# Kernel tuning notes

Hardware: AMD Instinct MI355X
Metric: run time of the kernel (lower is better)

The kernel has to match this reference:

```python
import jax, jax.numpy as jnp
import numpy as np

N_NODES = 100000
N_EDGES = 1000000
HID = 128


def setup_inputs() -> dict:
    key = jax.random.key(0)
    ks = jax.random.split(key, 13)
    s = 0.05  # small init scale for numerical sanity
    return {
        "z": jax.random.normal(ks[0], (N_NODES, HID), jnp.float32),
        "edge": jax.random.randint(ks[1], (N_EDGES, 2), 0, N_NODES, jnp.int64),
        # hadamard_mlp: Linear(HID -> HID//2), ReLU, Linear(HID//2 -> 1)
        "w_h1": jax.random.normal(ks[2], (HID // 2, HID), jnp.float32) * s,
        "b_h1": jax.random.normal(ks[3], (HID // 2,), jnp.float32) * s,
        "w_h2": jax.random.normal(ks[4], (1, HID // 2), jnp.float32) * s,
        "b_h2": jax.random.normal(ks[5], (1,), jnp.float32) * s,
        # concat_mlp: Linear(2*HID -> HID), ReLU, Linear(HID -> 1)
        "w_c1": jax.random.normal(ks[6], (HID, 2 * HID), jnp.float32) * s,
        "b_c1": jax.random.normal(ks[7], (HID,), jnp.float32) * s,
        "w_c2": jax.random.normal(ks[8], (1, HID), jnp.float32) * s,
        "b_c2": jax.random.normal(ks[9], (1,), jnp.float32) * s,
        # bilinear: weight [1, HID, HID], bias [1]
        "w_b": jax.random.normal(ks[10], (1, HID, HID), jnp.float32) * s,
        "b_b": jax.random.normal(ks[11], (1,), jnp.float32) * s,
        "strategy_weights": jnp.ones((3,), jnp.float32) / 3.0,
    }


def reference(z, edge, w_h1, b_h1, w_h2, b_h2, w_c1, b_c1, w_c2, b_c2,
              w_b, b_b, strategy_weights):
    src, dst = edge[:, 0], edge[:, 1]
    z_src = z[src]                      # [E, D] gather
    z_dst = z[dst]                      # [E, D] gather
    w = jax.nn.softmax(strategy_weights)

    # strategy 1: hadamard MLP (dropout is identity in eval)
    had = z_src * z_dst                 # [E, D]
    h = jax.nn.relu(jnp.einsum('ed,hd->eh', had, w_h1) + b_h1)
    score1 = (jnp.einsum('eh,oh->eo', h, w_h2) + b_h2)[:, 0]

    # strategy 2: concat MLP
    cat = jnp.concatenate([z_src, z_dst], axis=1)  # [E, 2D]
    c = jax.nn.relu(jnp.einsum('ed,hd->eh', cat, w_c1) + b_c1)
    score2 = (jnp.einsum('eh,oh->eo', c, w_c2) + b_c2)[:, 0]

    # strategy 3: bilinear  out_e = z_src_e^T W z_dst_e + b
    score3 = jnp.einsum('ed,df,ef->e', z_src, w_b[0], z_dst) + b_b[0]

    return w[0] * score1 + w[1] * score2 + w[2] * score3
```

## Files before the change

kernel.cpp:

```cpp
#include <hip/hip_runtime.h>
#include <hip/hip_bf16.h>

#define N_NODES 100000
#define N_EDGES 1000000
#define SRCB 384
#define DSTB 512
#define NB (N_EDGES / 16)

typedef float f32x4 __attribute__((ext_vector_type(4)));
typedef float f32x2 __attribute__((ext_vector_type(2)));
typedef _Float16 f16x8 __attribute__((ext_vector_type(8)));
typedef _Float16 f16x2 __attribute__((ext_vector_type(2)));

__device__ inline f16x8 pack8(float4 a, float4 b) {
    f16x8 o;
    o[0] = (_Float16)a.x; o[1] = (_Float16)a.y; o[2] = (_Float16)a.z; o[3] = (_Float16)a.w;
    o[4] = (_Float16)b.x; o[5] = (_Float16)b.y; o[6] = (_Float16)b.z; o[7] = (_Float16)b.w;
    return o;
}
__device__ inline void mfma16(f32x4& acc, f16x8 a, f16x8 b) {
    acc = __builtin_amdgcn_mfma_f32_16x16x32_f16(a, b, acc, 0, 0, 0);
}
__device__ inline float fdot2(f16x8 a, f16x8 b, int j2, float c) {
    f16x2 pa = { a[2 * j2], a[2 * j2 + 1] };
    f16x2 pb = { b[2 * j2], b[2 * j2 + 1] };
    return __builtin_amdgcn_fdot2(pa, pb, c, false);
}
__device__ inline unsigned char f2fp8(float v) {
    int p = __builtin_amdgcn_cvt_pk_fp8_f32(v, v, 0, false);
    return (unsigned char)(p & 0xff);
}

__global__ __launch_bounds__(256) void precomp_kernel(
    const float* __restrict__ z, const float* __restrict__ w_c1,
    const float* __restrict__ b_c1, const float* __restrict__ w_b,
    unsigned char* __restrict__ Ps8, unsigned char* __restrict__ Pd8)
{
    const int lane = threadIdx.x & 63;
    const int r = lane & 15, g = lane >> 4;
    const int wid = blockIdx.x * 4 + (threadIdx.x >> 6);
    const int ct = wid % 6;
    const int walker = wid / 6;
    const int nWalk = (gridDim.x * 4) / 6;
    if (walker >= nWalk) return;

    f16x8 bw[4][4];
#pragma unroll
    for (int nt = 0; nt < 4; ++nt) {
        const int c = ct * 64 + nt * 16 + r;
        const float* wrow;
        if (c < 128)       wrow = w_c1 + (size_t)c * 256;
        else if (c < 256)  wrow = w_c1 + (size_t)(c - 128) * 256 + 128;
        else               wrow = w_b + (size_t)(c - 256) * 128;
#pragma unroll
        for (int kk = 0; kk < 4; ++kk) {
            const int k0 = kk * 32 + g * 8;
            float4 f0 = *reinterpret_cast<const float4*>(wrow + k0);
            float4 f1 = *reinterpret_cast<const float4*>(wrow + k0 + 4);
            bw[nt][kk] = pack8(f0, f1);
        }
    }
    float bc1v[4] = {0.f, 0.f, 0.f, 0.f};
    if (ct < 2) {
#pragma unroll
        for (int nt = 0; nt < 4; ++nt) bc1v[nt] = b_c1[ct * 64 + nt * 16 + r];
    }

    for (int nb = walker; nb < N_NODES / 16; nb += nWalk) {
        const float* zp = z + (size_t)(nb * 16 + r) * 128;
        f32x4 acc[4] = {};
#pragma unroll
        for (int kk = 0; kk < 4; ++kk) {
            const int k0 = kk * 32 + g * 8;
            float4 z0 = *reinterpret_cast<const float4*>(zp + k0);
            float4 z1 = *reinterpret_cast<const float4*>(zp + k0 + 4);
            f16x8 a = pack8(z0, z1);
#pragma unroll
            for (int nt = 0; nt < 4; ++nt) mfma16(acc[nt], a, bw[nt][kk]);
        }
#pragma unroll
        for (int nt = 0; nt < 4; ++nt) {
#pragma unroll
            for (int rr = 0; rr < 4; ++rr) {
                const float v = acc[nt][rr] + bc1v[nt];
                const int node = nb * 16 + g * 4 + rr;
                const int c = ct * 64 + nt * 16 + r;
                if (ct < 2) {
                    Ps8[(size_t)node * SRCB + c] = f2fp8(v);
                } else if (ct < 4) {
                    Pd8[(size_t)node * DSTB + (c - 128)] = f2fp8(v);
                } else {
                    *reinterpret_cast<_Float16*>(
                        Pd8 + (size_t)node * DSTB + 128 + (size_t)(c - 256) * 2)
                        = (_Float16)v;
                }
            }
        }
    }
}

__global__ __launch_bounds__(256) void zb_kernel(const float* __restrict__ z,
                                                 unsigned char* __restrict__ Ps8,
                                                 unsigned char* __restrict__ Pd8)
{
    const int i = blockIdx.x * 256 + threadIdx.x;
    if (i >= N_NODES * 16) return;
    const int node = i >> 4, ch = i & 15;
    const float* zp = z + (size_t)node * 128 + ch * 8;
    float4 a = *reinterpret_cast<const float4*>(zp);
    float4 b = *reinterpret_cast<const float4*>(zp + 4);
    *reinterpret_cast<f16x8*>(Ps8 + (size_t)node * SRCB + 128 + ch * 16) = pack8(a, b);
    int w0 = __builtin_amdgcn_cvt_pk_fp8_f32(a.x, a.y, 0, false);
    w0 = __builtin_amdgcn_cvt_pk_fp8_f32(a.z, a.w, w0, true);
    int w1 = __builtin_amdgcn_cvt_pk_fp8_f32(b.x, b.y, 0, false);
    w1 = __builtin_amdgcn_cvt_pk_fp8_f32(b.z, b.w, w1, true);
    uint2 pk; pk.x = (unsigned)w0; pk.y = (unsigned)w1;
    *reinterpret_cast<uint2*>(Pd8 + (size_t)node * DSTB + 384 + ch * 8) = pk;
}

__global__ __launch_bounds__(256) void edge_kernel(
    const int2* __restrict__ edge2,
    const unsigned char* __restrict__ Ps8, const unsigned char* __restrict__ Pd8,
    const float* __restrict__ w_h1, const float* __restrict__ b_h1,
    const float* __restrict__ w_h2, const float* __restrict__ b_h2,
    const float* __restrict__ w_c2, const float* __restrict__ b_c2,
    const float* __restrict__ b_b, const float* __restrict__ sw,
    float* __restrict__ out)
{
    __shared__ f16x8 bwlds[1024];

    const int tid = threadIdx.x;
    for (int e = tid; e < 1024; e += 256) {
        const int r_ = e & 15, g_ = (e >> 4) & 3, kkf = (e >> 6) & 3, ntf = e >> 8;
        const float* wr = w_h1 + (size_t)(ntf * 16 + r_) * 128 + g_ * 32 + kkf * 8;
        float4 f0 = *reinterpret_cast<const float4*>(wr);
        float4 f1 = *reinterpret_cast<const float4*>(wr + 4);
        bwlds[e] = pack8(f0, f1);
    }
    __syncthreads();

    const int lane = tid & 63;
    const int r = lane & 15, g = lane >> 4;

    const float s0 = sw[0], s1 = sw[1], s2 = sw[2];
    const float mx = fmaxf(s0, fmaxf(s1, s2));
    const float e0 = __expf(s0 - mx), e1 = __expf(s1 - mx), e2 = __expf(s2 - mx);
    const float inv = 1.0f / (e0 + e1 + e2);
    const float W0 = e0 * inv, W1 = e1 * inv, W2 = e2 * inv;
    const float cbias = W0 * b_h2[0] + W1 * b_c2[0] + W2 * b_b[0];

    float bh1v[4], wh2v[4];
#pragma unroll
    for (int nt = 0; nt < 4; ++nt) {
        bh1v[nt] = b_h1[nt * 16 + r];
        wh2v[nt] = w_h2[nt * 16 + r] * W0;
    }
    f16x8 wc2r[4];
#pragma unroll
    for (int kk = 0; kk < 4; ++kk) {
        const int k0 = g * 32 + kk * 8;
        float4 f0 = *reinterpret_cast<const float4*>(w_c2 + k0);
        float4 f1 = *reinterpret_cast<const float4*>(w_c2 + k0 + 4);
        f0.x *= W1; f0.y *= W1; f0.z *= W1; f0.w *= W1;
        f1.x *= W1; f1.y *= W1; f1.z *= W1; f1.w *= W1;
        wc2r[kk] = pack8(f0, f1);
    }
    const f16x8* myb = bwlds + g * 16 + r;

    const int gwid = (blockIdx.x * blockDim.x + tid) >> 6;
    const int nW = (gridDim.x * blockDim.x) >> 6;
    const int rsel = r & 3;
    const int srcl = ((r >> 2) << 4) | r;

    int b = gwid;
    int2 sd = make_int2(0, 0);
    if (b < NB) sd = edge2[b * 16 + r];

    for (; b < NB; b += nW) {
        const int bn = b + nW;
        int2 sdn = sd;
        if (bn < NB) sdn = edge2[bn * 16 + r];

        const int base = b * 16;
        const unsigned char* ps = Ps8 + (size_t)sd.x * SRCB;
        const unsigned char* pd = Pd8 + (size_t)sd.y * DSTB;

        uint4 a16[2], b16[2], zq[2];
        f16x8 zs[4], yv[4];
        a16[0] = *reinterpret_cast<const uint4*>(ps + g * 32);
        a16[1] = *reinterpret_cast<const uint4*>(ps + g * 32 + 16);
        b16[0] = *reinterpret_cast<const uint4*>(pd + g * 32);
        b16[1] = *reinterpret_cast<const uint4*>(pd + g * 32 + 16);
        zq[0]  = *reinterpret_cast<const uint4*>(pd + 384 + g * 32);
        zq[1]  = *reinterpret_cast<const uint4*>(pd + 384 + g * 32 + 16);
#pragma unroll
        for (int kk = 0; kk < 4; ++kk) {
            const int of = g * 64 + kk * 16;
            zs[kk] = *reinterpret_cast<const f16x8*>(ps + 128 + of);
            yv[kk] = *reinterpret_cast<const f16x8*>(pd + 128 + of);
        }
        const unsigned zdw[8] = { zq[0].x, zq[0].y, zq[0].z, zq[0].w,
                                  zq[1].x, zq[1].y, zq[1].z, zq[1].w };

        f32x4 acc[4] = {};
#pragma unroll
        for (int kk = 0; kk < 4; ++kk) {
            f32x2 p0 = __builtin_amdgcn_cvt_pk_f32_fp8((int)zdw[2 * kk], false);
            f32x2 p1 = __builtin_amdgcn_cvt_pk_f32_fp8((int)zdw[2 * kk], true);
            f32x2 p2 = __builtin_amdgcn_cvt_pk_f32_fp8((int)zdw[2 * kk + 1], false);
            f32x2 p3 = __builtin_amdgcn_cvt_pk_f32_fp8((int)zdw[2 * kk + 1], true);
            f16x8 a;
            a[0] = (_Float16)((float)zs[kk][0] * p0.x);
            a[1] = (_Float16)((float)zs[kk][1] * p0.y);
            a[2] = (_Float16)((float)zs[kk][2] * p1.x);
            a[3] = (_Float16)((float)zs[kk][3] * p1.y);
            a[4] = (_Float16)((float)zs[kk][4] * p2.x);
            a[5] = (_Float16)((float)zs[kk][5] * p2.y);
            a[6] = (_Float16)((float)zs[kk][6] * p3.x);
            a[7] = (_Float16)((float)zs[kk][7] * p3.y);
            mfma16(acc[0], a, myb[(0 * 4 + kk) * 64]);
            mfma16(acc[1], a, myb[(1 * 4 + kk) * 64]);
            mfma16(acc[2], a, myb[(2 * 4 + kk) * 64]);
            mfma16(acc[3], a, myb[(3 * 4 + kk) * 64]);
        }
        float t4[4];
#pragma unroll
        for (int rr = 0; rr < 4; ++rr) {
            float s = 0.f;
#pragma unroll
            for (int nt = 0; nt < 4; ++nt)
                s = fmaf(fmaxf(acc[nt][rr] + bh1v[nt], 0.f), wh2v[nt], s);
            t4[rr] = s;
        }
#pragma unroll
        for (int mask = 1; mask <= 8; mask <<= 1) {
#pragma unroll
            for (int rr = 0; rr < 4; ++rr)
                t4[rr] += __shfl_xor(t4[rr], mask, 16);
        }
        float u = t4[0];
        if (rsel == 1) u = t4[1];
        if (rsel == 2) u = t4[2];
        if (rsel == 3) u = t4[3];
        const float sc1w = __shfl(u, srcl, 64);

        float sA = 0.f, sB = 0.f;
#pragma unroll
        for (int h = 0; h < 2; ++h) {
            const unsigned ax = a16[h].x, ay = a16[h].y, az = a16[h].z, aw = a16[h].w;
            const unsigned bx = b16[h].x, by = b16[h].y, bz = b16[h].z, bw_ = b16[h].w;
            f32x2 pa0 = __builtin_amdgcn_cvt_pk_f32_fp8((int)ax, false);
            f32x2 pa1 = __builtin_amdgcn_cvt_pk_f32_fp8((int)ax, true);
            f32x2 pa2 = __builtin_amdgcn_cvt_pk_f32_fp8((int)ay, false);
            f32x2 pa3 = __builtin_amdgcn_cvt_pk_f32_fp8((int)ay, true);
            f32x2 pa4 = __builtin_amdgcn_cvt_pk_f32_fp8((int)az, false);
            f32x2 pa5 = __builtin_amdgcn_cvt_pk_f32_fp8((int)az, true);
            f32x2 pa6 = __builtin_amdgcn_cvt_pk_f32_fp8((int)aw, false);
            f32x2 pa7 = __builtin_amdgcn_cvt_pk_f32_fp8((int)aw, true);
            f32x2 pb0 = __builtin_amdgcn_cvt_pk_f32_fp8((int)bx, false);
            f32x2 pb1 = __builtin_amdgcn_cvt_pk_f32_fp8((int)bx, true);
            f32x2 pb2 = __builtin_amdgcn_cvt_pk_f32_fp8((int)by, false);
            f32x2 pb3 = __builtin_amdgcn_cvt_pk_f32_fp8((int)by, true);
            f32x2 pb4 = __builtin_amdgcn_cvt_pk_f32_fp8((int)bz, false);
            f32x2 pb5 = __builtin_amdgcn_cvt_pk_f32_fp8((int)bz, true);
            f32x2 pb6 = __builtin_amdgcn_cvt_pk_f32_fp8((int)bw_, false);
            f32x2 pb7 = __builtin_amdgcn_cvt_pk_f32_fp8((int)bw_, true);
            const f16x8 w0 = wc2r[2 * h], w1 = wc2r[2 * h + 1];
            sA = fmaf(fmaxf(pa0.x + pb0.x, 0.f), (float)w0[0], sA);
            sA = fmaf(fmaxf(pa0.y + pb0.y, 0.f), (float)w0[1], sA);
            sA = fmaf(fmaxf(pa1.x + pb1.x, 0.f), (float)w0[2], sA);
            sA = fmaf(fmaxf(pa1.y + pb1.y, 0.f), (float)w0[3], sA);
            sA = fmaf(fmaxf(pa2.x + pb2.x, 0.f), (float)w0[4], sA);
            sA = fmaf(fmaxf(pa2.y + pb2.y, 0.f), (float)w0[5], sA);
            sA = fmaf(fmaxf(pa3.x + pb3.x, 0.f), (float)w0[6], sA);
            sA = fmaf(fmaxf(pa3.y + pb3.y, 0.f), (float)w0[7], sA);
            sA = fmaf(fmaxf(pa4.x + pb4.x, 0.f), (float)w1[0], sA);
            sA = fmaf(fmaxf(pa4.y + pb4.y, 0.f), (float)w1[1], sA);
            sA = fmaf(fmaxf(pa5.x + pb5.x, 0.f), (float)w1[2], sA);
            sA = fmaf(fmaxf(pa5.y + pb5.y, 0.f), (float)w1[3], sA);
            sA = fmaf(fmaxf(pa6.x + pb6.x, 0.f), (float)w1[4], sA);
            sA = fmaf(fmaxf(pa6.y + pb6.y, 0.f), (float)w1[5], sA);
            sA = fmaf(fmaxf(pa7.x + pb7.x, 0.f), (float)w1[6], sA);
            sA = fmaf(fmaxf(pa7.y + pb7.y, 0.f), (float)w1[7], sA);
        }
#pragma unroll
        for (int kk = 0; kk < 4; ++kk)
#pragma unroll
            for (int j2 = 0; j2 < 4; ++j2)
                sB = fdot2(zs[kk], yv[kk], j2, sB);

        sA += __shfl_xor(sA, 16, 64);
        sA += __shfl_xor(sA, 32, 64);
        sB += __shfl_xor(sB, 16, 64);
        sB += __shfl_xor(sB, 32, 64);

        const float res = sc1w + sA + fmaf(W2, sB, cbias);
        if (lane < 16) out[base + lane] = res;
        sd = sdn;
    }
}

__global__ __launch_bounds__(256) void fused_fallback(
    const float* __restrict__ z, const int* __restrict__ edge,
    const float* __restrict__ w_h1, const float* __restrict__ b_h1,
    const float* __restrict__ w_h2, const float* __restrict__ b_h2,
    const float* __restrict__ w_c1, const float* __restrict__ b_c1,
    const float* __restrict__ w_c2, const float* __restrict__ b_c2,
    const float* __restrict__ w_b, const float* __restrict__ b_b,
    const float* __restrict__ sw, float* __restrict__ out)
{
    __shared__ float zbuf[4][256];
    const int lane = threadIdx.x & 63;
    const int w = threadIdx.x >> 6;
    const int gw = blockIdx.x * 4 + w;
    const int nw = gridDim.x * 4;

    const float s0 = sw[0], s1 = sw[1], s2 = sw[2];
    const float mx = fmaxf(s0, fmaxf(s1, s2));
    const float e0 = __expf(s0 - mx), e1 = __expf(s1 - mx), e2 = __expf(s2 - mx);
    const float inv = 1.0f / (e0 + e1 + e2);
    const float W0 = e0 * inv, W1 = e1 * inv, W2 = e2 * inv;
    const float cbias = W0 * b_h2[0] + W1 * b_c2[0] + W2 * b_b[0];

    for (int e = gw; e < N_EDGES; e += nw) {
        const int src = edge[2 * e], dst = edge[2 * e + 1];
        const float zs0 = z[(size_t)src * 128 + lane];
        const float zs1 = z[(size_t)src * 128 + 64 + lane];
        const float zd0 = z[(size_t)dst * 128 + lane];
        const float zd1 = z[(size_t)dst * 128 + 64 + lane];
        zbuf[w][lane] = zs0; zbuf[w][64 + lane] = zs1;
        zbuf[w][128 + lane] = zd0; zbuf[w][192 + lane] = zd1;
        asm volatile("s_waitcnt lgkmcnt(0)" ::: "memory");

        float h = 0.f;
        const float* whr = w_h1 + (size_t)lane * 128;
        for (int d = 0; d < 128; ++d)
            h = fmaf(zbuf[w][d] * zbuf[w][128 + d], whr[d], h);
        float sc1 = fmaxf(h + b_h1[lane], 0.f) * w_h2[lane];

        float c0 = 0.f, c1 = 0.f;
        const float* w0r = w_c1 + (size_t)lane * 256;
        const float* w1r = w_c1 + (size_t)(lane + 64) * 256;
        for (int d = 0; d < 256; ++d) {
            const float cat = zbuf[w][d];
            c0 = fmaf(cat, w0r[d], c0);
            c1 = fmaf(cat, w1r[d], c1);
        }
        float sc2 = fmaxf(c0 + b_c1[lane], 0.f) * w_c2[lane]
                  + fmaxf(c1 + b_c1[lane + 64], 0.f) * w_c2[lane + 64];

        float t0 = 0.f, t1 = 0.f;
        const float* wb0 = w_b + (size_t)lane * 128;
        const float* wb1 = w_b + (size_t)(lane + 64) * 128;
        for (int f = 0; f < 128; ++f) {
            const float zdf = zbuf[w][128 + f];
            t0 = fmaf(wb0[f], zdf, t0);
            t1 = fmaf(wb1[f], zdf, t1);
        }
        float sc3 = zs0 * t0 + zs1 * t1;

        float v = fmaf(W0, sc1, fmaf(W1, sc2, W2 * sc3));
#pragma unroll
        for (int m = 1; m < 64; m <<= 1) v += __shfl_xor(v, m, 64);
        if (lane == 0) out[e] = v + cbias;
    }
}

extern "C" void kernel_launch(void* const* d_in, const int* in_sizes, int n_in,
                              void* d_out, int out_size, void* d_ws, size_t ws_size,
                              hipStream_t stream)
{
    const float* z    = (const float*)d_in[0];
    const int*   edge = (const int*)d_in[1];
    const float* w_h1 = (const float*)d_in[2];
    const float* b_h1 = (const float*)d_in[3];
    const float* w_h2 = (const float*)d_in[4];
    const float* b_h2 = (const float*)d_in[5];
    const float* w_c1 = (const float*)d_in[6];
    const float* b_c1 = (const float*)d_in[7];
    const float* w_c2 = (const float*)d_in[8];
    const float* b_c2 = (const float*)d_in[9];
    const float* w_b  = (const float*)d_in[10];
    const float* b_b  = (const float*)d_in[11];
    const float* sw   = (const float*)d_in[12];
    float* outp = (float*)d_out;

    const size_t szSrc = (size_t)N_NODES * SRCB;
    const size_t szDst = (size_t)N_NODES * DSTB;
    const size_t need  = szSrc + szDst;

    if (ws_size >= need) {
        unsigned char* Ps8 = (unsigned char*)d_ws;
        unsigned char* Pd8 = (unsigned char*)d_ws + szSrc;
        hipLaunchKernelGGL(precomp_kernel, dim3(768), dim3(256), 0, stream,
                           z, w_c1, b_c1, w_b, Ps8, Pd8);
        hipLaunchKernelGGL(zb_kernel, dim3((N_NODES * 16 + 255) / 256), dim3(256),
                           0, stream, z, Ps8, Pd8);
        hipLaunchKernelGGL(edge_kernel, dim3(1024), dim3(256), 0, stream,
                           (const int2*)edge, Ps8, Pd8, w_h1, b_h1, w_h2, b_h2,
                           w_c2, b_c2, b_b, sw, outp);
    } else {
        hipLaunchKernelGGL(fused_fallback, dim3(4096), dim3(256), 0, stream,
                           z, edge, w_h1, b_h1, w_h2, b_h2, w_c1, b_c1,
                           w_c2, b_c2, w_b, b_b, sw, outp);
    }
}
```

Before: 203.3 us.

## Fuse z conversion into precompute kernel and stage weights in LDS

Merges the separate zb_kernel (fp16/fp8 copies of z) into the precompute kernel and restructures it. Each wave now loads a 16-node z tile once per phase and computes three column tiles from weights staged in shared memory, rather than having six waves each reload the same z rows with weights held in registers. This cuts redundant z reads and removes one kernel launch. The cost is 48KB of LDS per block, two sync phases, and z being read twice (once per phase).

```diff
diff --git a/kernel.cpp b/kernel.cpp
--- a/kernel.cpp
+++ b/kernel.cpp
@@ -6,6 +6,7 @@
 #define SRCB 384
 #define DSTB 512
 #define NB (N_EDGES / 16)
+#define NCHUNK (N_NODES / 16)
 
 typedef float f32x4 __attribute__((ext_vector_type(4)));
 typedef float f32x2 __attribute__((ext_vector_type(2)));
@@ -31,91 +32,100 @@
     return (unsigned char)(p & 0xff);
 }
 
-__global__ __launch_bounds__(256) void precomp_kernel(
+__global__ __launch_bounds__(512) void precomp_kernel(
     const float* __restrict__ z, const float* __restrict__ w_c1,
     const float* __restrict__ b_c1, const float* __restrict__ w_b,
     unsigned char* __restrict__ Ps8, unsigned char* __restrict__ Pd8)
 {
-    const int lane = threadIdx.x & 63;
+    __shared__ f16x8 wlds[3072];
+
+    const int tid = threadIdx.x;
+    const int w = tid >> 6;
+    const int lane = tid & 63;
     const int r = lane & 15, g = lane >> 4;
-    const int wid = blockIdx.x * 4 + (threadIdx.x >> 6);
-    const int ct = wid % 6;
-    const int walker = wid / 6;
-    const int nWalk = (gridDim.x * 4) / 6;
-    if (walker >= nWalk) return;
-
-    f16x8 bw[4][4];
-#pragma unroll
-    for (int nt = 0; nt < 4; ++nt) {
-        const int c = ct * 64 + nt * 16 + r;
-        const float* wrow;
-        if (c < 128)       wrow = w_c1 + (size_t)c * 256;
-        else if (c < 256)  wrow = w_c1 + (size_t)(c - 128) * 256 + 128;
-        else               wrow = w_b + (size_t)(c - 256) * 128;
-#pragma unroll
-        for (int kk = 0; kk < 4; ++kk) {
-            const int k0 = kk * 32 + g * 8;
+    const int gw = blockIdx.x * 8 + w;
+    const int nW = gridDim.x * 8;
+
+    float bc1v[2][4];
+#pragma unroll
+    for (int t = 0; t < 2; ++t)
+#pragma unroll
+        for (int nt = 0; nt < 4; ++nt)
+            bc1v[t][nt] = b_c1[t * 64 + nt * 16 + r];
+
+    for (int phase = 0; phase < 2; ++phase) {
+        if (phase) __syncthreads();
+        for (int i = tid; i < 3072; i += 512) {
+            const int r_ = i & 15, g_ = (i >> 4) & 3, kk = (i >> 6) & 3;
+            const int nt = (i >> 8) & 3, t = i >> 10;
+            const int c = (phase * 3 + t) * 64 + nt * 16 + r_;
+            const float* wrow;
+            if (c < 128)       wrow = w_c1 + (size_t)c * 256;
+            else if (c < 256)  wrow = w_c1 + (size_t)(c - 128) * 256 + 128;
+            else               wrow = w_b + (size_t)(c - 256) * 128;
+            const int k0 = kk * 32 + g_ * 8;
             float4 f0 = *reinterpret_cast<const float4*>(wrow + k0);
             float4 f1 = *reinterpret_cast<const float4*>(wrow + k0 + 4);
-            bw[nt][kk] = pack8(f0, f1);
-        }
-    }
-    float bc1v[4] = {0.f, 0.f, 0.f, 0.f};
-    if (ct < 2) {
-#pragma unroll
-        for (int nt = 0; nt < 4; ++nt) bc1v[nt] = b_c1[ct * 64 + nt * 16 + r];
-    }
-
-    for (int nb = walker; nb < N_NODES / 16; nb += nWalk) {
-        const float* zp = z + (size_t)(nb * 16 + r) * 128;
-        f32x4 acc[4] = {};
-#pragma unroll
-        for (int kk = 0; kk < 4; ++kk) {
-            const int k0 = kk * 32 + g * 8;
-            float4 z0 = *reinterpret_cast<const float4*>(zp + k0);
-            float4 z1 = *reinterpret_cast<const float4*>(zp + k0 + 4);
-            f16x8 a = pack8(z0, z1);
-#pragma unroll
-            for (int nt = 0; nt < 4; ++nt) mfma16(acc[nt], a, bw[nt][kk]);
-        }
-#pragma unroll
-        for (int nt = 0; nt < 4; ++nt) {
-#pragma unroll
-            for (int rr = 0; rr < 4; ++rr) {
-                const float v = acc[nt][rr] + bc1v[nt];
-                const int node = nb * 16 + g * 4 + rr;
-                const int c = ct * 64 + nt * 16 + r;
-                if (ct < 2) {
-                    Ps8[(size_t)node * SRCB + c] = f2fp8(v);
-                } else if (ct < 4) {
-                    Pd8[(size_t)node * DSTB + (c - 128)] = f2fp8(v);
-                } else {
-                    *reinterpret_cast<_Float16*>(
-                        Pd8 + (size_t)node * DSTB + 128 + (size_t)(c - 256) * 2)
-                        = (_Float16)v;
+            wlds[i] = pack8(f0, f1);
+        }
+        __syncthreads();
+
+        const f16x8* myw = wlds + g * 16 + r;
+
+        for (int nb = gw; nb < NCHUNK; nb += nW) {
+            const int node_r = nb * 16 + r;
+            const float* zp = z + (size_t)node_r * 128;
+            f16x8 a[4];
+#pragma unroll
+            for (int kk = 0; kk < 4; ++kk) {
+                const int k0 = kk * 32 + g * 8;
+                float4 z0 = *reinterpret_cast<const float4*>(zp + k0);
+                float4 z1 = *reinterpret_cast<const float4*>(zp + k0 + 4);
+                a[kk] = pack8(z0, z1);
+                if (phase == 0) {
+                    *reinterpret_cast<f16x8*>(
+                        Ps8 + (size_t)node_r * SRCB + 128 + k0 * 2) = a[kk];
+                    int q0 = __builtin_amdgcn_cvt_pk_fp8_f32(z0.x, z0.y, 0, false);
+                    q0 = __builtin_amdgcn_cvt_pk_fp8_f32(z0.z, z0.w, q0, true);
+                    int q1 = __builtin_amdgcn_cvt_pk_fp8_f32(z1.x, z1.y, 0, false);
+                    q1 = __builtin_amdgcn_cvt_pk_fp8_f32(z1.z, z1.w, q1, true);
+                    uint2 pk; pk.x = (unsigned)q0; pk.y = (unsigned)q1;
+                    *reinterpret_cast<uint2*>(
+                        Pd8 + (size_t)node_r * DSTB + 384 + k0) = pk;
                 }
             }
-        }
-    }
-}
-
-__global__ __launch_bounds__(256) void zb_kernel(const float* __restrict__ z,
-                                                 unsigned char* __restrict__ Ps8,
-                                                 unsigned char* __restrict__ Pd8)
-{
-    const int i = blockIdx.x * 256 + threadIdx.x;
-    if (i >= N_NODES * 16) return;
-    const int node = i >> 4, ch = i & 15;
-    const float* zp = z + (size_t)node * 128 + ch * 8;
-    float4 a = *reinterpret_cast<const float4*>(zp);
-    float4 b = *reinterpret_cast<const float4*>(zp + 4);
-    *reinterpret_cast<f16x8*>(Ps8 + (size_t)node * SRCB + 128 + ch * 16) = pack8(a, b);
-    int w0 = __builtin_amdgcn_cvt_pk_fp8_f32(a.x, a.y, 0, false);
-    w0 = __builtin_amdgcn_cvt_pk_fp8_f32(a.z, a.w, w0, true);
-    int w1 = __builtin_amdgcn_cvt_pk_fp8_f32(b.x, b.y, 0, false);
-    w1 = __builtin_amdgcn_cvt_pk_fp8_f32(b.z, b.w, w1, true);
-    uint2 pk; pk.x = (unsigned)w0; pk.y = (unsigned)w1;
-    *reinterpret_cast<uint2*>(Pd8 + (size_t)node * DSTB + 384 + ch * 8) = pk;
+#pragma unroll
+            for (int t = 0; t < 3; ++t) {
+                const int ct = phase * 3 + t;
+                f32x4 acc[4] = {};
+#pragma unroll
+                for (int kk = 0; kk < 4; ++kk) {
+#pragma unroll
+                    for (int nt = 0; nt < 4; ++nt)
+                        mfma16(acc[nt], a[kk], myw[((t * 4 + nt) * 4 + kk) * 64]);
+                }
+#pragma unroll
+                for (int nt = 0; nt < 4; ++nt) {
+#pragma unroll
+                    for (int rr = 0; rr < 4; ++rr) {
+                        const int node = nb * 16 + g * 4 + rr;
+                        const int c = ct * 64 + nt * 16 + r;
+                        float v = acc[nt][rr];
+                        if (ct < 2) {
+                            v += bc1v[ct][nt];
+                            Ps8[(size_t)node * SRCB + c] = f2fp8(v);
+                        } else if (ct < 4) {
+                            Pd8[(size_t)node * DSTB + (c - 128)] = f2fp8(v);
+                        } else {
+                            *reinterpret_cast<_Float16*>(
+                                Pd8 + (size_t)node * DSTB + 128
+                                    + (size_t)(c - 256) * 2) = (_Float16)v;
+                        }
+                    }
+                }
+            }
+        }
+    }
 }
 
 __global__ __launch_bounds__(256) void edge_kernel(
@@ -392,10 +402,8 @@
     if (ws_size >= need) {
         unsigned char* Ps8 = (unsigned char*)d_ws;
         unsigned char* Pd8 = (unsigned char*)d_ws + szSrc;
-        hipLaunchKernelGGL(precomp_kernel, dim3(768), dim3(256), 0, stream,
+        hipLaunchKernelGGL(precomp_kernel, dim3(512), dim3(512), 0, stream,
                            z, w_c1, b_c1, w_b, Ps8, Pd8);
-        hipLaunchKernelGGL(zb_kernel, dim3((N_NODES * 16 + 255) / 256), dim3(256),
-                           0, stream, z, Ps8, Pd8);
         hipLaunchKernelGGL(edge_kernel, dim3(1024), dim3(256), 0, stream,
                            (const int2*)edge, Ps8, Pd8, w_h1, b_h1, w_h2, b_h2,
                            w_c2, b_c2, b_b, sw, outp);
```

Result: faster. 188.7 us (-7.2%).
